# Kernel optimization log

Measured on AMD Instinct MI355X. Metric: run time of the kernel, lower is better.

Reference implementation:

```python
import jax, jax.numpy as jnp
import numpy as np

K = 3
EPS = 1e-5


def _lc(x, W, b):
    """Locally connected layer: per-output-location unshared weights.
    x: (B,C,H,Wd); W: (O,C,oh,ow,k,k); b: (O,oh,ow) -> (B,O,oh,ow)"""
    B, C, H, Wd = x.shape
    oh, ow = H - K + 1, Wd - K + 1
    # patches: (B,C,oh,ow,k,k) -- small, avoids torch's (B,O,C,oh,ow,k,k) blowup
    patches = jnp.stack(
        [jnp.stack([x[:, :, i:i + oh, j:j + ow] for j in range(K)], axis=-1)
         for i in range(K)], axis=-2)
    return jnp.einsum('bchwij,ochwij->bohw', patches, W) + b[None]


def _bn(x, g, b):
    # training-mode batch norm (batch statistics, biased variance)
    m = x.mean(axis=(0, 2, 3), keepdims=True)
    v = x.var(axis=(0, 2, 3), keepdims=True)
    return g[None, :, None, None] * (x - m) * jax.lax.rsqrt(v + EPS) + b[None, :, None, None]


def setup_inputs() -> dict:
    key = jax.random.key(0)
    ks = jax.random.split(key, 6)
    B = 1024
    return {
        'x':   jax.random.normal(ks[0], (B, 1, 16, 16), jnp.float32),
        'W1':  jax.random.normal(ks[1], (16, 1, 14, 14, 3, 3), jnp.float32),
        'b1':  jnp.zeros((16, 14, 14), jnp.float32),
        'g1':  jnp.ones((16,), jnp.float32),
        'be1': jnp.zeros((16,), jnp.float32),
        'W2':  jax.random.normal(ks[2], (32, 16, 12, 12, 3, 3), jnp.float32),
        'b2':  jnp.zeros((32, 12, 12), jnp.float32),
        'g2':  jnp.ones((32,), jnp.float32),
        'be2': jnp.zeros((32,), jnp.float32),
        'W3':  jax.random.normal(ks[3], (64, 32, 10, 10, 3, 3), jnp.float32),
        'b3':  jnp.zeros((64, 10, 10), jnp.float32),
        'g3':  jnp.ones((64,), jnp.float32),
        'be3': jnp.zeros((64,), jnp.float32),
        'fcW': jax.random.normal(ks[4], (10, 6400), jnp.float32) * 0.01,
        'fcb': jnp.zeros((10,), jnp.float32),
    }


def reference(x, W1, b1, g1, be1, W2, b2, g2, be2, W3, b3, g3, be3, fcW, fcb):
    h = jax.nn.relu(_bn(_lc(x, W1, b1), g1, be1))       # (B,16,14,14)
    h = jax.nn.relu(_bn(_lc(h, W2, b2), g2, be2))       # (B,32,12,12)
    h = jnp.tanh(_bn(_lc(h, W3, b3), g3, be3))          # (B,64,10,10)
    h = h.reshape(h.shape[0], -1)                        # (B,6400)
    return h @ fcW.T + fcb                               # (B,10)
```

## Files before the change

kernel.cpp:

```cpp
#include <hip/hip_runtime.h>

#define EPS 1e-5f

typedef _Float16 f16x8 __attribute__((ext_vector_type(8)));
typedef _Float16 f16x4 __attribute__((ext_vector_type(4)));
typedef float f32x4 __attribute__((ext_vector_type(4)));

#define XT_OFF    0u
#define ACT1_OFF  262144u
#define ACT2_OFF  1867776u
#define ACT3_OFF  4227072u
#define W2H_OFF   7503872u
#define W3H_OFF   7872512u
#define FP_OFF    9598976u
#define ACC_OFF   10622976u

__global__ __launch_bounds__(256) void k_prep(const float* __restrict__ W2,
                                              const float* __restrict__ W3,
                                              const float* __restrict__ x,
                                              _Float16* __restrict__ W2h,
                                              _Float16* __restrict__ W3h,
                                              float* __restrict__ xT,
                                              float* __restrict__ acc) {
    int gb = blockIdx.x, tid = threadIdx.x;
    __shared__ float tile[32][33];
    int tx = tid & 31, ty = tid >> 5;
    if (gb < 656) {
        int tR = gb / 41, tC = gb % 41;
        int oc0 = tR * 32, pp0 = tC * 32;
#pragma unroll
        for (int r = 0; r < 4; r++) {
            int col = pp0 + tx;
            if (col < 1296) tile[ty + 8 * r][tx] = W2[(size_t)(oc0 + ty + 8 * r) * 1296 + col];
        }
        __syncthreads();
#pragma unroll
        for (int r = 0; r < 4; r++) {
            int pr = pp0 + ty + 8 * r;
            if (pr < 1296) {
                int p = pr / 9, pos = pr - 9 * p;
                W2h[(size_t)(p * 10 + pos) * 512 + oc0 + tx] = (_Float16)tile[tx][ty + 8 * r];
            }
        }
        return;
    }
    if (gb < 692) {
        if (gb == 656) {
#pragma unroll
            for (int r = 0; r < 8; r++) acc[r * 256 + tid] = 0.f;
        }
        int idx = (gb - 656) * 256 + tid;
        int p = idx >> 6, ocv = idx & 63;
        f16x8 z = {(_Float16)0.f, (_Float16)0.f, (_Float16)0.f, (_Float16)0.f,
                   (_Float16)0.f, (_Float16)0.f, (_Float16)0.f, (_Float16)0.f};
        *(f16x8*)(W2h + (size_t)(p * 10 + 9) * 512 + ocv * 8) = z;
        return;
    }
    if (gb < 2548) {
        int t = gb - 692;
        int tR = t / 29, tC = t % 29;
        int oc0 = tR * 32, pp0 = tC * 32;
#pragma unroll
        for (int r = 0; r < 4; r++) {
            int col = pp0 + tx;
            if (col < 900) tile[ty + 8 * r][tx] = W3[(size_t)(oc0 + ty + 8 * r) * 900 + col];
        }
        __syncthreads();
#pragma unroll
        for (int r = 0; r < 4; r++) {
            int pr = pp0 + ty + 8 * r;
            if (pr < 900) W3h[(size_t)pr * 2048 + oc0 + tx] = (_Float16)tile[tx][ty + 8 * r];
        }
        return;
    }
    {
        int t = gb - 2548;
        float* t17 = &tile[0][0];
        int tx4 = tid & 15, ty4 = tid >> 4;
        int p0 = (t & 15) * 16, b0 = (t >> 4) * 16;
        t17[ty4 * 17 + tx4] = x[(b0 + ty4) * 256 + p0 + tx4];
        __syncthreads();
        xT[(p0 + ty4) * 1024 + b0 + tx4] = t17[tx4 * 17 + ty4];
    }
}

__global__ __launch_bounds__(256) void k_lc1(const float* __restrict__ xT,
                                             const float* __restrict__ W1,
                                             const float* __restrict__ b1,
                                             _Float16* __restrict__ act1h,
                                             float* __restrict__ acc) {
    int bid = blockIdx.x;
    int rep = bid & 7;
    int wg = (bid & 7) * 98 + (bid >> 3);
    int p = wg >> 2;
    int i = p / 14, j = p % 14;
    int tid = threadIdx.x;
    int b = (wg & 3) * 256 + tid;
    __shared__ float wS[144], bS[16];
    __shared__ float red[256 * 33];
    __shared__ float pp[4 * 33];
    if (tid < 144) { int o = tid / 9, k = tid % 9; wS[tid] = W1[(o * 196 + p) * 9 + k]; }
    if (tid < 16) bS[tid] = b1[tid * 196 + p];
    __syncthreads();
    float xv[9];
#pragma unroll
    for (int di = 0; di < 3; di++)
#pragma unroll
        for (int dj = 0; dj < 3; dj++)
            xv[di * 3 + dj] = xT[((i + di) * 16 + (j + dj)) * 1024 + b];
    float accv[16];
#pragma unroll
    for (int o = 0; o < 16; o++) {
        float acc2_ = bS[o];
#pragma unroll
        for (int k = 0; k < 9; k++) acc2_ += wS[o * 9 + k] * xv[k];
        accv[o] = acc2_;
    }
    f16x8 lo, hi;
#pragma unroll
    for (int e = 0; e < 8; e++) { lo[e] = (_Float16)accv[e]; hi[e] = (_Float16)accv[8 + e]; }
    _Float16* dst = act1h + ((size_t)(p * 1024 + b)) * 16;
    *(f16x8*)dst = lo;
    *(f16x8*)(dst + 8) = hi;
#pragma unroll
    for (int o = 0; o < 16; o++) {
        red[tid * 33 + o] = accv[o];
        red[tid * 33 + 16 + o] = accv[o] * accv[o];
    }
    __syncthreads();
    {
        int w = tid >> 6, lane = tid & 63, v = lane & 31, h = lane >> 5;
        int rbase = w * 64 + h * 32;
        float ssum = 0.f;
#pragma unroll
        for (int k = 0; k < 32; k++) ssum += red[(rbase + k) * 33 + v];
        ssum += __shfl_down(ssum, 32);
        if (h == 0) pp[w * 33 + v] = ssum;
    }
    __syncthreads();
    if (tid < 32) {
        float t4 = pp[tid] + pp[33 + tid] + pp[66 + tid] + pp[99 + tid];
        atomicAdd(acc + rep * 256 + tid, t4);
    }
}

__global__ __launch_bounds__(256) void k_lc2m(const _Float16* __restrict__ act1h,
                                              const _Float16* __restrict__ W2h,
                                              const float* __restrict__ b2,
                                              const float* __restrict__ acc,
                                              const float* __restrict__ g1,
                                              const float* __restrict__ be1,
                                              _Float16* __restrict__ act2h,
                                              float* __restrict__ accw) {
    int bid = blockIdx.x;
    int rep = bid & 7;
    int wg = (bid & 7) * 72 + (bid >> 3);
    int p = wg >> 2, i = p / 12, j = p % 12;
    int tid = threadIdx.x, wv = tid >> 6, lane = tid & 63, n = lane & 15, quad = lane >> 4;
    int bbase = (wg & 3) * 256 + wv * 64;
    __shared__ _Float16 wL[10 * 512];
    for (int idx = tid; idx < 640; idx += 256)
        *(f16x8*)(wL + idx * 8) = *(const f16x8*)(W2h + (size_t)p * 5120 + idx * 8);
    const float invN1 = 1.f / (1024.f * 196.f);
    f16x8 a8, c8;
#pragma unroll
    for (int e = 0; e < 8; e++) {
        int ch = (quad & 1) * 8 + e;
        float s = 0.f, q = 0.f;
#pragma unroll
        for (int r = 0; r < 8; r++) { s += acc[r * 256 + ch]; q += acc[r * 256 + 16 + ch]; }
        float m = s * invN1, var = q * invN1 - m * m;
        float rr = rsqrtf(var + EPS);
        float av = g1[ch] * rr;
        a8[e] = (_Float16)av;
        c8[e] = (_Float16)(be1[ch] - m * av);
    }
    __syncthreads();
    f32x4 accm[2][4] = {};
#pragma unroll
    for (int t = 0; t < 5; t++) {
        int posA = 2 * t + (quad >> 1);
        int posB = posA > 8 ? 8 : posA;
        int ip = (i + posB / 3) * 14 + (j + posB % 3);
        f16x8 afr[2];
#pragma unroll
        for (int ot = 0; ot < 2; ot++)
            afr[ot] = *(const f16x8*)(wL + posA * 512 + (ot * 16 + n) * 16 + (quad & 1) * 8);
#pragma unroll
        for (int nt = 0; nt < 4; nt++) {
            f16x8 xv = *(const f16x8*)(act1h + ((size_t)(ip * 1024 + bbase + nt * 16 + n)) * 16 + (quad & 1) * 8);
#pragma unroll
            for (int e = 0; e < 8; e++) {
                _Float16 v = xv[e] * a8[e] + c8[e];
                xv[e] = v > (_Float16)0.f ? v : (_Float16)0.f;
            }
#pragma unroll
            for (int ot = 0; ot < 2; ot++)
                accm[ot][nt] = __builtin_amdgcn_mfma_f32_16x16x32_f16(afr[ot], xv, accm[ot][nt], 0, 0, 0);
        }
    }
    float s_[8] = {}, q_[8] = {};
#pragma unroll
    for (int ot = 0; ot < 2; ot++) {
        float bias[4];
#pragma unroll
        for (int r = 0; r < 4; r++) bias[r] = b2[(ot * 16 + quad * 4 + r) * 144 + p];
#pragma unroll
        for (int nt = 0; nt < 4; nt++) {
            int b = bbase + nt * 16 + n;
            f16x4 st;
#pragma unroll
            for (int r = 0; r < 4; r++) {
                float v = accm[ot][nt][r] + bias[r];
                st[r] = (_Float16)v;
                s_[ot * 4 + r] += v; q_[ot * 4 + r] += v * v;
            }
            *(f16x4*)(act2h + ((size_t)(p * 1024 + b)) * 32 + ot * 16 + quad * 4) = st;
        }
    }
    __shared__ float red[64 * 65];
#pragma unroll
    for (int u = 0; u < 8; u++) {
        int o = (u >> 2) * 16 + quad * 4 + (u & 3);
        red[(2 * o) * 65 + wv * 16 + n] = s_[u];
        red[(2 * o + 1) * 65 + wv * 16 + n] = q_[u];
    }
    __syncthreads();
    if (tid < 64) {
        const float* row = red + tid * 65;
        float t0 = 0.f;
#pragma unroll
        for (int c = 0; c < 64; c++) t0 += row[c];
        atomicAdd(accw + rep * 256 + 32 + (tid & 1) * 32 + (tid >> 1), t0);
    }
}

__global__ __launch_bounds__(256) void k_lc3m(const _Float16* __restrict__ act2h,
                                              const _Float16* __restrict__ W3h,
                                              const float* __restrict__ b3,
                                              const float* __restrict__ acc,
                                              const float* __restrict__ g2,
                                              const float* __restrict__ be2,
                                              _Float16* __restrict__ act3h,
                                              float* __restrict__ accw) {
    int bid = blockIdx.x;
    int rep = bid & 7;
    int wg = (bid & 7) * 50 + (bid >> 3);
    int p = wg >> 2, i = p / 10, j = p % 10;
    int tid = threadIdx.x, wv = tid >> 6, lane = tid & 63, n = lane & 15, quad = lane >> 4;
    int bbase = (wg & 3) * 256 + wv * 64;
    __shared__ _Float16 wL[9 * 2048];
    for (int idx = tid; idx < 2304; idx += 256)
        *(f16x8*)(wL + idx * 8) = *(const f16x8*)(W3h + (size_t)p * 18432 + idx * 8);
    const float invN2 = 1.f / (1024.f * 144.f);
    f16x8 a8, c8;
#pragma unroll
    for (int e = 0; e < 8; e++) {
        int ch = quad * 8 + e;
        float s = 0.f, q = 0.f;
#pragma unroll
        for (int r = 0; r < 8; r++) { s += acc[r * 256 + 32 + ch]; q += acc[r * 256 + 64 + ch]; }
        float m = s * invN2, var = q * invN2 - m * m;
        float rr = rsqrtf(var + EPS);
        float av = g2[ch] * rr;
        a8[e] = (_Float16)av;
        c8[e] = (_Float16)(be2[ch] - m * av);
    }
    __syncthreads();
    f32x4 accm[4][4] = {};
#pragma unroll
    for (int pos = 0; pos < 9; pos++) {
        int ip = (i + pos / 3) * 12 + (j + pos % 3);
        f16x8 afr[4];
#pragma unroll
        for (int ot = 0; ot < 4; ot++)
            afr[ot] = *(const f16x8*)(wL + pos * 2048 + (ot * 16 + n) * 32 + quad * 8);
#pragma unroll
        for (int nt = 0; nt < 4; nt++) {
            f16x8 xv = *(const f16x8*)(act2h + ((size_t)(ip * 1024 + bbase + nt * 16 + n)) * 32 + quad * 8);
#pragma unroll
            for (int e = 0; e < 8; e++) {
                _Float16 v = xv[e] * a8[e] + c8[e];
                xv[e] = v > (_Float16)0.f ? v : (_Float16)0.f;
            }
#pragma unroll
            for (int ot = 0; ot < 4; ot++)
                accm[ot][nt] = __builtin_amdgcn_mfma_f32_16x16x32_f16(afr[ot], xv, accm[ot][nt], 0, 0, 0);
        }
    }
    float s_[16] = {}, q_[16] = {};
#pragma unroll
    for (int ot = 0; ot < 4; ot++) {
        float bias[4];
#pragma unroll
        for (int r = 0; r < 4; r++) bias[r] = b3[(ot * 16 + quad * 4 + r) * 100 + p];
#pragma unroll
        for (int nt = 0; nt < 4; nt++) {
            int b = bbase + nt * 16 + n;
            f16x4 st;
#pragma unroll
            for (int r = 0; r < 4; r++) {
                float v = accm[ot][nt][r] + bias[r];
                st[r] = (_Float16)v;
                s_[ot * 4 + r] += v; q_[ot * 4 + r] += v * v;
            }
            *(f16x4*)(act3h + ((size_t)(p * 1024 + b)) * 64 + ot * 16 + quad * 4) = st;
        }
    }
    __shared__ float red[128 * 65];
#pragma unroll
    for (int u = 0; u < 16; u++) {
        int o = (u >> 2) * 16 + quad * 4 + (u & 3);
        red[(2 * o) * 65 + wv * 16 + n] = s_[u];
        red[(2 * o + 1) * 65 + wv * 16 + n] = q_[u];
    }
    __syncthreads();
    if (tid < 128) {
        const float* row = red + tid * 65;
        float t0 = 0.f;
#pragma unroll
        for (int c = 0; c < 64; c++) t0 += row[c];
        atomicAdd(accw + rep * 256 + 96 + (tid & 1) * 64 + (tid >> 1), t0);
    }
}

__global__ __launch_bounds__(256) void k_fc(const _Float16* __restrict__ act3h,
                                            const float* __restrict__ fcW,
                                            const float* __restrict__ acc,
                                            const float* __restrict__ g3,
                                            const float* __restrict__ be3,
                                            float* __restrict__ fpart) {
    int p = blockIdx.y;
    int tid = threadIdx.x;
    int b = blockIdx.x * 256 + tid;
    __shared__ float wS[640], aS[64], cS[64];
    for (int idx = tid; idx < 640; idx += 256) {
        int o = idx / 10, jj = idx % 10;
        wS[idx] = fcW[jj * 6400 + o * 100 + p];
    }
    if (tid < 64) {
        const float invN3 = 1.f / (1024.f * 100.f);
        float s = 0.f, q = 0.f;
#pragma unroll
        for (int r = 0; r < 8; r++) { s += acc[r * 256 + 96 + tid]; q += acc[r * 256 + 160 + tid]; }
        float m = s * invN3, var = q * invN3 - m * m;
        float rr = rsqrtf(var + EPS);
        float av = g3[tid] * rr;
        aS[tid] = av; cS[tid] = be3[tid] - m * av;
    }
    __syncthreads();
    float accv[10];
#pragma unroll
    for (int jj = 0; jj < 10; jj++) accv[jj] = 0.f;
    const _Float16* src = act3h + ((size_t)(p * 1024 + b)) * 64;
    for (int o8 = 0; o8 < 8; o8++) {
        f16x8 xv = *(const f16x8*)(src + o8 * 8);
#pragma unroll
        for (int e = 0; e < 8; e++) {
            int o = o8 * 8 + e;
            float v = fmaf(aS[o], (float)xv[e], cS[o]);
            float e2 = __expf(2.f * v);
            v = 1.f - 2.f / (e2 + 1.f);
#pragma unroll
            for (int jj = 0; jj < 10; jj++) accv[jj] = fmaf(wS[o * 10 + jj], v, accv[jj]);
        }
    }
#pragma unroll
    for (int jj = 0; jj < 10; jj++) fpart[((size_t)p * 10 + jj) * 1024 + b] = accv[jj];
}

__global__ __launch_bounds__(256) void k_fc_reduce(const float* __restrict__ fpart,
                                                   const float* __restrict__ fcb,
                                                   float* __restrict__ out) {
    int idx = blockIdx.x * 256 + threadIdx.x;
    int jj = idx >> 10, b = idx & 1023;
    float acc = fcb[jj];
    for (int p = 0; p < 100; p++) acc += fpart[(p * 10 + jj) * 1024 + b];
    out[b * 10 + jj] = acc;
}

extern "C" void kernel_launch(void* const* d_in, const int* in_sizes, int n_in,
                              void* d_out, int out_size, void* d_ws, size_t ws_size,
                              hipStream_t stream) {
    const float* x   = (const float*)d_in[0];
    const float* W1  = (const float*)d_in[1];
    const float* b1  = (const float*)d_in[2];
    const float* g1  = (const float*)d_in[3];
    const float* be1 = (const float*)d_in[4];
    const float* W2  = (const float*)d_in[5];
    const float* b2  = (const float*)d_in[6];
    const float* g2  = (const float*)d_in[7];
    const float* be2 = (const float*)d_in[8];
    const float* W3  = (const float*)d_in[9];
    const float* b3  = (const float*)d_in[10];
    const float* g3  = (const float*)d_in[11];
    const float* be3 = (const float*)d_in[12];
    const float* fcW = (const float*)d_in[13];
    const float* fcb = (const float*)d_in[14];
    float* out = (float*)d_out;
    float* ws = (float*)d_ws;

    float* xT    = ws + XT_OFF;
    _Float16* act1h = (_Float16*)(ws + ACT1_OFF);
    _Float16* act2h = (_Float16*)(ws + ACT2_OFF);
    _Float16* act3h = (_Float16*)(ws + ACT3_OFF);
    _Float16* W2h   = (_Float16*)(ws + W2H_OFF);
    _Float16* W3h   = (_Float16*)(ws + W3H_OFF);
    float* fp   = ws + FP_OFF;
    float* acc  = ws + ACC_OFF;

    k_prep<<<3572, 256, 0, stream>>>(W2, W3, x, W2h, W3h, xT, acc);
    k_lc1<<<784, 256, 0, stream>>>(xT, W1, b1, act1h, acc);
    k_lc2m<<<576, 256, 0, stream>>>(act1h, W2h, b2, acc, g1, be1, act2h, acc);
    k_lc3m<<<400, 256, 0, stream>>>(act2h, W3h, b3, acc, g2, be2, act3h, acc);
    k_fc<<<dim3(4, 100), 256, 0, stream>>>(act3h, fcW, acc, g3, be3, fp);
    k_fc_reduce<<<40, 256, 0, stream>>>(fp, fcb, out);
}
```

Baseline: 145.0 us.

## Replace FC partial-sum reduce kernel with atomics and widen stat replicas

Drops the separate fc_reduce kernel: the output is seeded with the bias inside the prep kernel, and each FC block atomically adds its partial sums straight into the output. BN statistic atomics are spread over 16 replica slots instead of 8 to reduce contention. The LC2/LC3 kernels reuse the weight shared-memory buffer for the reduction scratch, which cuts LDS use and may raise occupancy. The cost is 100-way atomic contention per output element and a summation order that is no longer deterministic.

```diff
diff --git a/kernel.cpp b/kernel.cpp
--- a/kernel.cpp
+++ b/kernel.cpp
@@ -12,7 +12,6 @@
 #define ACT3_OFF  4227072u
 #define W2H_OFF   7503872u
 #define W3H_OFF   7872512u
-#define FP_OFF    9598976u
 #define ACC_OFF   10622976u
 
 __global__ __launch_bounds__(256) void k_prep(const float* __restrict__ W2,
@@ -21,7 +20,9 @@
                                               _Float16* __restrict__ W2h,
                                               _Float16* __restrict__ W3h,
                                               float* __restrict__ xT,
-                                              float* __restrict__ acc) {
+                                              float* __restrict__ acc,
+                                              const float* __restrict__ fcb,
+                                              float* __restrict__ out) {
     int gb = blockIdx.x, tid = threadIdx.x;
     __shared__ float tile[32][33];
     int tx = tid & 31, ty = tid >> 5;
@@ -47,7 +48,7 @@
     if (gb < 692) {
         if (gb == 656) {
 #pragma unroll
-            for (int r = 0; r < 8; r++) acc[r * 256 + tid] = 0.f;
+            for (int r = 0; r < 16; r++) acc[r * 256 + tid] = 0.f;
         }
         int idx = (gb - 656) * 256 + tid;
         int p = idx >> 6, ocv = idx & 63;
@@ -73,7 +74,7 @@
         }
         return;
     }
-    {
+    if (gb < 3572) {
         int t = gb - 2548;
         float* t17 = &tile[0][0];
         int tx4 = tid & 15, ty4 = tid >> 4;
@@ -81,6 +82,11 @@
         t17[ty4 * 17 + tx4] = x[(b0 + ty4) * 256 + p0 + tx4];
         __syncthreads();
         xT[(p0 + ty4) * 1024 + b0 + tx4] = t17[tx4 * 17 + ty4];
+        return;
+    }
+    {
+        int idx = (gb - 3572) * 256 + tid;
+        out[idx] = fcb[idx % 10];
     }
 }
 
@@ -90,7 +96,7 @@
                                              _Float16* __restrict__ act1h,
                                              float* __restrict__ acc) {
     int bid = blockIdx.x;
-    int rep = bid & 7;
+    int rep = bid & 15;
     int wg = (bid & 7) * 98 + (bid >> 3);
     int p = wg >> 2;
     int i = p / 14, j = p % 14;
@@ -111,10 +117,10 @@
     float accv[16];
 #pragma unroll
     for (int o = 0; o < 16; o++) {
-        float acc2_ = bS[o];
-#pragma unroll
-        for (int k = 0; k < 9; k++) acc2_ += wS[o * 9 + k] * xv[k];
-        accv[o] = acc2_;
+        float a_ = bS[o];
+#pragma unroll
+        for (int k = 0; k < 9; k++) a_ += wS[o * 9 + k] * xv[k];
+        accv[o] = a_;
     }
     f16x8 lo, hi;
 #pragma unroll
@@ -153,12 +159,13 @@
                                               _Float16* __restrict__ act2h,
                                               float* __restrict__ accw) {
     int bid = blockIdx.x;
-    int rep = bid & 7;
+    int rep = bid & 15;
     int wg = (bid & 7) * 72 + (bid >> 3);
     int p = wg >> 2, i = p / 12, j = p % 12;
     int tid = threadIdx.x, wv = tid >> 6, lane = tid & 63, n = lane & 15, quad = lane >> 4;
     int bbase = (wg & 3) * 256 + wv * 64;
-    __shared__ _Float16 wL[10 * 512];
+    __shared__ float sh[64 * 65];
+    _Float16* wL = (_Float16*)sh;
     for (int idx = tid; idx < 640; idx += 256)
         *(f16x8*)(wL + idx * 8) = *(const f16x8*)(W2h + (size_t)p * 5120 + idx * 8);
     const float invN1 = 1.f / (1024.f * 196.f);
@@ -168,7 +175,7 @@
         int ch = (quad & 1) * 8 + e;
         float s = 0.f, q = 0.f;
 #pragma unroll
-        for (int r = 0; r < 8; r++) { s += acc[r * 256 + ch]; q += acc[r * 256 + 16 + ch]; }
+        for (int r = 0; r < 16; r++) { s += acc[r * 256 + ch]; q += acc[r * 256 + 16 + ch]; }
         float m = s * invN1, var = q * invN1 - m * m;
         float rr = rsqrtf(var + EPS);
         float av = g1[ch] * rr;
@@ -199,6 +206,7 @@
                 accm[ot][nt] = __builtin_amdgcn_mfma_f32_16x16x32_f16(afr[ot], xv, accm[ot][nt], 0, 0, 0);
         }
     }
+    __syncthreads();
     float s_[8] = {}, q_[8] = {};
 #pragma unroll
     for (int ot = 0; ot < 2; ot++) {
@@ -218,16 +226,15 @@
             *(f16x4*)(act2h + ((size_t)(p * 1024 + b)) * 32 + ot * 16 + quad * 4) = st;
         }
     }
-    __shared__ float red[64 * 65];
 #pragma unroll
     for (int u = 0; u < 8; u++) {
         int o = (u >> 2) * 16 + quad * 4 + (u & 3);
-        red[(2 * o) * 65 + wv * 16 + n] = s_[u];
-        red[(2 * o + 1) * 65 + wv * 16 + n] = q_[u];
+        sh[(2 * o) * 65 + wv * 16 + n] = s_[u];
+        sh[(2 * o + 1) * 65 + wv * 16 + n] = q_[u];
     }
     __syncthreads();
     if (tid < 64) {
-        const float* row = red + tid * 65;
+        const float* row = sh + tid * 65;
         float t0 = 0.f;
 #pragma unroll
         for (int c = 0; c < 64; c++) t0 += row[c];
@@ -244,12 +251,13 @@
                                               _Float16* __restrict__ act3h,
                                               float* __restrict__ accw) {
     int bid = blockIdx.x;
-    int rep = bid & 7;
+    int rep = bid & 15;
     int wg = (bid & 7) * 50 + (bid >> 3);
     int p = wg >> 2, i = p / 10, j = p % 10;
     int tid = threadIdx.x, wv = tid >> 6, lane = tid & 63, n = lane & 15, quad = lane >> 4;
     int bbase = (wg & 3) * 256 + wv * 64;
     __shared__ _Float16 wL[9 * 2048];
+    float* red = (float*)wL;
     for (int idx = tid; idx < 2304; idx += 256)
         *(f16x8*)(wL + idx * 8) = *(const f16x8*)(W3h + (size_t)p * 18432 + idx * 8);
     const float invN2 = 1.f / (1024.f * 144.f);
@@ -259,7 +267,7 @@
         int ch = quad * 8 + e;
         float s = 0.f, q = 0.f;
 #pragma unroll
-        for (int r = 0; r < 8; r++) { s += acc[r * 256 + 32 + ch]; q += acc[r * 256 + 64 + ch]; }
+        for (int r = 0; r < 16; r++) { s += acc[r * 256 + 32 + ch]; q += acc[r * 256 + 64 + ch]; }
         float m = s * invN2, var = q * invN2 - m * m;
         float rr = rsqrtf(var + EPS);
         float av = g2[ch] * rr;
@@ -288,6 +296,7 @@
                 accm[ot][nt] = __builtin_amdgcn_mfma_f32_16x16x32_f16(afr[ot], xv, accm[ot][nt], 0, 0, 0);
         }
     }
+    __syncthreads();
     float s_[16] = {}, q_[16] = {};
 #pragma unroll
     for (int ot = 0; ot < 4; ot++) {
@@ -307,7 +316,6 @@
             *(f16x4*)(act3h + ((size_t)(p * 1024 + b)) * 64 + ot * 16 + quad * 4) = st;
         }
     }
-    __shared__ float red[128 * 65];
 #pragma unroll
     for (int u = 0; u < 16; u++) {
         int o = (u >> 2) * 16 + quad * 4 + (u & 3);
@@ -329,7 +337,7 @@
                                             const float* __restrict__ acc,
                                             const float* __restrict__ g3,
                                             const float* __restrict__ be3,
-                                            float* __restrict__ fpart) {
+                                            float* __restrict__ out) {
     int p = blockIdx.y;
     int tid = threadIdx.x;
     int b = blockIdx.x * 256 + tid;
@@ -342,7 +350,7 @@
         const float invN3 = 1.f / (1024.f * 100.f);
         float s = 0.f, q = 0.f;
 #pragma unroll
-        for (int r = 0; r < 8; r++) { s += acc[r * 256 + 96 + tid]; q += acc[r * 256 + 160 + tid]; }
+        for (int r = 0; r < 16; r++) { s += acc[r * 256 + 96 + tid]; q += acc[r * 256 + 160 + tid]; }
         float m = s * invN3, var = q * invN3 - m * m;
         float rr = rsqrtf(var + EPS);
         float av = g3[tid] * rr;
@@ -366,17 +374,7 @@
         }
     }
 #pragma unroll
-    for (int jj = 0; jj < 10; jj++) fpart[((size_t)p * 10 + jj) * 1024 + b] = accv[jj];
-}
-
-__global__ __launch_bounds__(256) void k_fc_reduce(const float* __restrict__ fpart,
-                                                   const float* __restrict__ fcb,
-                                                   float* __restrict__ out) {
-    int idx = blockIdx.x * 256 + threadIdx.x;
-    int jj = idx >> 10, b = idx & 1023;
-    float acc = fcb[jj];
-    for (int p = 0; p < 100; p++) acc += fpart[(p * 10 + jj) * 1024 + b];
-    out[b * 10 + jj] = acc;
+    for (int jj = 0; jj < 10; jj++) atomicAdd(out + b * 10 + jj, accv[jj]);
 }
 
 extern "C" void kernel_launch(void* const* d_in, const int* in_sizes, int n_in,
@@ -406,13 +404,11 @@
     _Float16* act3h = (_Float16*)(ws + ACT3_OFF);
     _Float16* W2h   = (_Float16*)(ws + W2H_OFF);
     _Float16* W3h   = (_Float16*)(ws + W3H_OFF);
-    float* fp   = ws + FP_OFF;
     float* acc  = ws + ACC_OFF;
 
-    k_prep<<<3572, 256, 0, stream>>>(W2, W3, x, W2h, W3h, xT, acc);
+    k_prep<<<3612, 256, 0, stream>>>(W2, W3, x, W2h, W3h, xT, acc, fcb, out);
     k_lc1<<<784, 256, 0, stream>>>(xT, W1, b1, act1h, acc);
     k_lc2m<<<576, 256, 0, stream>>>(act1h, W2h, b2, acc, g1, be1, act2h, acc);
     k_lc3m<<<400, 256, 0, stream>>>(act2h, W3h, b3, acc, g2, be2, act3h, acc);
-    k_fc<<<dim3(4, 100), 256, 0, stream>>>(act3h, fcW, acc, g3, be3, fp);
-    k_fc_reduce<<<40, 256, 0, stream>>>(fp, fcb, out);
-}
+    k_fc<<<dim3(4, 100), 256, 0, stream>>>(act3h, fcW, acc, g3, be3, out);
+}
```

New measurement: 204.2 us. 1.41x slower.
